# Optimization experiments

Measured on AMD Instinct MI355X. Metric: run time of the kernel, lower is better.

## Reference

```python
import jax, jax.numpy as jnp
import numpy as np

DIM = 70      # voxel grid side
NE = 6        # element channels
B = 8         # batch
TARGET = 29   # TARGET_NUM in source


def _xavier(key, shape, fan_in, fan_out):
    lim = float(np.sqrt(6.0 / (fan_in + fan_out)))
    return jax.random.uniform(key, shape, jnp.float32, -lim, lim)


def setup_inputs() -> dict:
    key = jax.random.key(0)
    ks = jax.random.split(key, 12)
    # Sparse binary occupancy grid: ~34 atoms per channel per molecule.
    x = (jax.random.uniform(ks[0], (B, NE, DIM, DIM, DIM)) < 1e-4).astype(jnp.float32)
    sigma = 2.0 * jnp.ones((NE,), jnp.float32)
    k3 = 3 * 3 * 3
    conv1_w = _xavier(ks[1], (32, NE, 3, 3, 3), NE * k3, 32 * k3)
    conv2_w = _xavier(ks[2], (64, 32, 3, 3, 3), 32 * k3, 64 * k3)
    conv3_w = _xavier(ks[3], (128, 64, 3, 3, 3), 64 * k3, 128 * k3)
    conv4_w = _xavier(ks[4], (256, 128, 3, 3, 3), 128 * k3, 256 * k3)
    conv1_b = jnp.full((32,), 0.01, jnp.float32)
    conv2_b = jnp.full((64,), 0.01, jnp.float32)
    conv3_b = jnp.full((128,), 0.01, jnp.float32)
    conv4_b = jnp.full((256,), 0.01, jnp.float32)
    fc1_w = _xavier(ks[5], (1024, 2048), 2048, 1024)
    fc1_b = jnp.full((1024,), 0.01, jnp.float32)
    fc2_w = _xavier(ks[6], (TARGET, 1024), 1024, TARGET)
    fc2_b = jax.random.uniform(ks[7], (TARGET,), jnp.float32, -1.0 / 32.0, 1.0 / 32.0)
    return dict(x=x, sigma=sigma,
                conv1_w=conv1_w, conv1_b=conv1_b, conv2_w=conv2_w, conv2_b=conv2_b,
                conv3_w=conv3_w, conv3_b=conv3_b, conv4_w=conv4_w, conv4_b=conv4_b,
                fc1_w=fc1_w, fc1_b=fc1_b, fc2_w=fc2_w, fc2_b=fc2_b)


def _blur(x, sigma):
    # Faithful to source: Gaussian centered at raw voxel INDICES (x0,y0,z0 from
    # nonzero()) but evaluated on SHIFTED coords arange(-dim/2, dim/2).
    # Separable Gaussian -> three 1D contractions instead of per-atom loops.
    coords = jnp.arange(DIM, dtype=jnp.float32) - DIM / 2.0   # -35 .. 34
    idx = jnp.arange(DIM, dtype=jnp.float32)                   # 0 .. 69
    d2 = (coords[:, None] - idx[None, :]) ** 2                 # [70,70]
    G = jnp.exp(-d2[None, :, :] / (2.0 * sigma[:, None, None] ** 2))  # [e,out,in]
    mask = (x != 0).astype(x.dtype)                            # [b,e,i,j,k]
    t = jnp.einsum('beijk,eai->beajk', mask, G)
    t = jnp.einsum('beajk,epj->beapk', t, G)
    cube = jnp.einsum('beapk,eqk->beapq', t, G)                # [b,e,70,70,70]
    return cube


def _conv3d(h, w, b):
    y = jax.lax.conv_general_dilated(h, w, (1, 1, 1), 'VALID',
                                     dimension_numbers=('NCDHW', 'OIDHW', 'NCDHW'))
    return y + b[None, :, None, None, None]


def _pool(h):
    return jax.lax.reduce_window(h, -jnp.inf, jax.lax.max,
                                 (1, 1, 2, 2, 2), (1, 1, 2, 2, 2), 'VALID')


def reference(x, sigma, conv1_w, conv1_b, conv2_w, conv2_b, conv3_w, conv3_b,
              conv4_w, conv4_b, fc1_w, fc1_b, fc2_w, fc2_b):
    h = _blur(x, sigma)
    h = jax.nn.relu(_pool(_conv3d(h, conv1_w, conv1_b)))
    h = jax.nn.relu(_pool(_conv3d(h, conv2_w, conv2_b)))
    h = jax.nn.relu(_pool(_conv3d(h, conv3_w, conv3_b)))
    h = jax.nn.relu(_pool(_conv3d(h, conv4_w, conv4_b)))  # [B,256,2,2,2]
    v = h.reshape(x.shape[0], -1)                          # [B,2048]
    y1 = jax.nn.relu(v @ fc1_w.T + fc1_b)
    y2 = y1 @ fc2_w.T + fc2_b                              # [B,29]
    return y2
```

## Files before the change

kernel.cpp:

```cpp
#include <hip/hip_runtime.h>
#include <hip/hip_bf16.h>

#define DIMV 70
#define NEL 6
#define BATCH 8

typedef unsigned short u16;
typedef unsigned int u32;
typedef __bf16 bf16x8 __attribute__((ext_vector_type(8)));
typedef short short8v __attribute__((ext_vector_type(8)));
typedef float f32x4 __attribute__((ext_vector_type(4)));

__device__ __forceinline__ u16 f2bf(float f) {
  __hip_bfloat16 h = __float2bfloat16(f);
  return __builtin_bit_cast(u16, h);
}
__device__ __forceinline__ float bf2f(u16 u) {
  unsigned int x = ((unsigned int)u) << 16;
  return __builtin_bit_cast(float, x);
}

__global__ __launch_bounds__(256) void k_zero(float* __restrict__ p, int n4) {
  int i = blockIdx.x * 256 + threadIdx.x;
  if (i < n4) ((float4*)p)[i] = make_float4(0.f, 0.f, 0.f, 0.f);
}

__global__ __launch_bounds__(256) void k_scan(const float* __restrict__ x,
                                              int* __restrict__ cnt,
                                              int* __restrict__ lists) {
  const int N4 = (BATCH * NEL * DIMV * DIMV * DIMV) / 4;
  int i = blockIdx.x * 256 + threadIdx.x;
  if (i >= N4) return;
  float4 v = ((const float4*)x)[i];
  int ch = i / 85750;
  int local = 4 * i - ch * 343000;
  float f[4] = {v.x, v.y, v.z, v.w};
#pragma unroll
  for (int k = 0; k < 4; ++k) {
    if (f[k] != 0.f) {
      int slot = atomicAdd(&cnt[ch], 1);
      if (slot < 512) lists[ch * 512 + slot] = local + k;
    }
  }
}

__global__ __launch_bounds__(256) void k_gather(const int* __restrict__ cnt,
                                                const int* __restrict__ lists,
                                                const float* __restrict__ sigma,
                                                u32* __restrict__ cube, int b0) {
  const int z = blockIdx.x;
  const int bl = blockIdx.y / NEL;
  const int e = blockIdx.y % NEL;
  const int chG = (b0 + bl) * NEL + e;
  const int tid = threadIdx.x;
  float sg = sigma[e];
  float inv2s2 = 1.f / (2.f * sg * sg);

  __shared__ int s_n;
  __shared__ int s_idx[512];
  __shared__ float s_wz[512];
  __shared__ float s_wy[32 * 70];
  __shared__ float s_wx[32 * 70];

  if (tid == 0) s_n = 0;
  __syncthreads();
  int n = min(cnt[chG], 512);
  for (int t = tid; t < n; t += 256) {
    int idx = lists[chG * 512 + t];
    int i0 = idx / 4900;
    float d = (float)(z - 35 - i0);
    float wz = expf(-d * d * inv2s2);
    if (wz > 1e-30f) {
      int s = atomicAdd(&s_n, 1);
      s_idx[s] = idx;
      s_wz[s] = wz;
    }
  }
  __syncthreads();
  int m = s_n;

  float acc[20];
#pragma unroll
  for (int k = 0; k < 20; ++k) acc[k] = 0.f;

  for (int t0 = 0; t0 < m; t0 += 32) {
    int tn = min(32, m - t0);
    __syncthreads();
    for (int u = tid; u < tn * 70; u += 256) {
      int t = u / 70, pos = u % 70;
      int idx = s_idx[t0 + t];
      int j0 = (idx / 70) % 70, k0 = idx % 70;
      float dy = (float)(pos - 35 - j0);
      float dx = (float)(pos - 35 - k0);
      s_wy[t * 70 + pos] = s_wz[t0 + t] * expf(-dy * dy * inv2s2);
      s_wx[t * 70 + pos] = expf(-dx * dx * inv2s2);
    }
    __syncthreads();
#pragma unroll
    for (int k = 0; k < 20; ++k) {
      int v = tid + k * 256;
      if (v < 4900) {
        int y = v / 70, xx = v % 70;
        float a = 0.f;
        for (int t = 0; t < tn; ++t)
          a = fmaf(s_wy[t * 70 + y], s_wx[t * 70 + xx], a);
        acc[k] += a;
      }
    }
  }
  size_t base = ((size_t)(bl * NEL + e) * DIMV + z) * 4900;
#pragma unroll
  for (int k = 0; k < 20; ++k) {
    int v = tid + k * 256;
    if (v < 4900) {
      float val = acc[k];
      u16 hi = f2bf(val);
      u16 lo = f2bf(val - bf2f(hi));
      cube[base + v] = ((u32)hi << 16) | (u32)lo;
    }
  }
}

__global__ __launch_bounds__(256) void k_pack_c1d(const float* __restrict__ w,
                                                  u16* __restrict__ Ah,
                                                  u16* __restrict__ Al) {
  int idx = blockIdx.x * 256 + threadIdx.x;
  if (idx >= 32 * 224) return;
  int o = idx / 224, k = idx % 224;
  int kk = k >> 5, r = k & 31;
  int g = r >> 3, e = r & 7;
  int off = 4 * kk + g;
  u16 h = 0, l = 0;
  if (off < 27 && e < 6) {
    float wv = w[(o * 6 + e) * 27 + off];
    u16 hi = f2bf(wv);
    h = hi;
    l = f2bf(wv - bf2f(hi));
  }
  Ah[idx] = h;
  Al[idx] = l;
}

__global__ __launch_bounds__(256) void k_pack_s(const float* __restrict__ w,
                                                u16* __restrict__ A,
                                                int CINL, int COUT) {
  int K2 = CINL * 81;
  int idx = blockIdx.x * 256 + threadIdx.x;
  if (idx >= COUT * K2) return;
  int o = idx / K2, k = idx % K2;
  int kb = k >> 5, r = k & 31;
  int g = r >> 3, e = r & 7;
  int kk = kb % 27;
  int t = kb / 27;
  int snum = CINL >> 5;
  int sub = t % snum, s = t / snum;
  int c = sub * 32 + 8 * g + e;
  float wv = w[(o * CINL + c) * 27 + kk];
  u16 hi = f2bf(wv);
  A[idx] = (s == 2) ? f2bf(wv - bf2f(hi)) : hi;
}

__global__ __launch_bounds__(256) void k_conv1(
    const u16* __restrict__ Ah, const u16* __restrict__ Al,
    const u32* __restrict__ cube, const float* __restrict__ bias,
    float* __restrict__ out, int b0) {
  __shared__ __align__(16) u16 Thi[1120 * 8];
  __shared__ __align__(16) u16 Tlo[1120 * 8];
  const int tid = threadIdx.x;
  const int wave = tid >> 6, lane = tid & 63;
  const int n = lane & 15, g = lane >> 4;
  const int py = blockIdx.x % 34, pz = blockIdx.x / 34;
  const int blb = blockIdx.y, bG = blb + b0;

  u32* thw = (u32*)Thi;
  u32* tlw = (u32*)Tlo;
  for (int i = tid; i < 4480; i += 256) {
    int j = i & 3, pos = i >> 2;
    int xx = pos % 70, line = pos / 70;
    int z = 2 * pz + (line >> 2), y = 2 * py + (line & 3);
    u32 a = 0, b2 = 0;
    if (j < 3) {
      size_t p0 = (((size_t)(blb * 6 + 2 * j) * 70 + z) * 70 + y) * 70 + xx;
      a = cube[p0];
      b2 = cube[p0 + 343000];
    }
    thw[pos * 4 + j] = (a >> 16) | (b2 & 0xFFFF0000u);
    tlw[pos * 4 + j] = (a & 0xFFFFu) | (b2 << 16);
  }
  __syncthreads();

  const int rc = wave;
  f32x4 acc[2][5] = {};
  for (int kk = 0; kk < 7; ++kk) {
    bf16x8 a0[2], a2[2];
#pragma unroll
    for (int mt = 0; mt < 2; ++mt) {
      const u16* bp = (const u16*)0;
      a0[mt] = __builtin_bit_cast(
          bf16x8, *(const short8v*)(Ah + (size_t)(mt * 16 + n) * 224 + kk * 32 + 8 * g));
      a2[mt] = __builtin_bit_cast(
          bf16x8, *(const short8v*)(Al + (size_t)(mt * 16 + n) * 224 + kk * 32 + 8 * g));
      (void)bp;
    }
    int off = min(4 * kk + g, 26);
    int dz = off / 9, dy = (off / 3) % 3, dx = off % 3;
    int line = ((rc >> 1) + dz) * 4 + (rc & 1) + dy;
#pragma unroll
    for (int nt = 0; nt < 5; ++nt) {
      int x_in = nt * 16 + n + dx;
      if (x_in > 69) x_in = 69;
      int cell = (line * 70 + x_in) * 8;
      bf16x8 bh = __builtin_bit_cast(bf16x8, *(const short8v*)&Thi[cell]);
      bf16x8 bl = __builtin_bit_cast(bf16x8, *(const short8v*)&Tlo[cell]);
#pragma unroll
      for (int mt = 0; mt < 2; ++mt) {
        acc[mt][nt] = __builtin_amdgcn_mfma_f32_16x16x32_bf16(a0[mt], bh, acc[mt][nt], 0, 0, 0);
        acc[mt][nt] = __builtin_amdgcn_mfma_f32_16x16x32_bf16(a2[mt], bh, acc[mt][nt], 0, 0, 0);
        acc[mt][nt] = __builtin_amdgcn_mfma_f32_16x16x32_bf16(a0[mt], bl, acc[mt][nt], 0, 0, 0);
      }
    }
  }
  __syncthreads();
  float* Pb = (float*)Thi;
#pragma unroll
  for (int mt = 0; mt < 2; ++mt) {
#pragma unroll
    for (int nt = 0; nt < 5; ++nt) {
#pragma unroll
      for (int r = 0; r < 4; ++r) {
        float v = acc[mt][nt][r];
        float v2 = fmaxf(v, __shfl_xor(v, 1));
        int o = mt * 16 + 4 * g + r;
        int px = (nt * 16 + n) >> 1;
        if (!(n & 1) && px < 34) Pb[(wave * 32 + o) * 34 + px] = v2;
      }
    }
  }
  __syncthreads();
  for (int t = tid; t < 1088; t += 256) {
    int o = t / 34, px = t % 34;
    float m = fmaxf(fmaxf(Pb[t], Pb[1088 + t]), fmaxf(Pb[2176 + t], Pb[3264 + t]));
    float rv = fmaxf(m + bias[o], 0.f);
    out[((((size_t)bG * 32 + o) * 34 + pz) * 34 + py) * 34 + px] = rv;
  }
}

template <int CINL, int COUT, int DIN, int WAVES, int MREP, int XT>
__global__ __launch_bounds__(WAVES * 64) void k_conv_s(
    const u16* __restrict__ Apack, const float* __restrict__ in,
    const float* __restrict__ bias, float* __restrict__ out) {
  constexpr int DP = (DIN - 2) / 2;
  constexpr int SNUM = CINL / 32;
  constexpr int K2 = 81 * CINL;
  __shared__ __align__(16) u16 T[16 * DIN * 32];

  const int tid = threadIdx.x;
  const int wave = tid >> 6, lane = tid & 63;
  const int n = lane & 15, g = lane >> 4;
  const int py = blockIdx.x % DP, pz = blockIdx.x / DP;
  const int b = blockIdx.y;

  f32x4 acc[MREP][4][XT] = {};

  for (int ph = 0; ph < 2; ++ph) {
    for (int sub = 0; sub < SNUM; ++sub) {
      if (ph + sub) __syncthreads();
      const int E2 = 16 * DIN * 16;
      for (int i = tid; i < E2; i += WAVES * 64) {
        int xx = i % DIN;
        int t2 = i / DIN;
        int jp = t2 & 15;
        int line = t2 >> 4;
        int z = 2 * pz + (line >> 2), y = 2 * py + (line & 3);
        int c = sub * 32 + 2 * jp;
        size_t base = (((size_t)(b * CINL + c) * DIN + z) * DIN + y) * DIN + xx;
        float v0 = in[base];
        float v1 = in[base + (size_t)DIN * DIN * DIN];
        u16 h0 = f2bf(v0), h1 = f2bf(v1);
        u16 a0 = ph ? f2bf(v0 - bf2f(h0)) : h0;
        u16 a1 = ph ? f2bf(v1 - bf2f(h1)) : h1;
        int byte = (line * DIN + xx) * 64 + (((jp >> 2) ^ (xx & 3)) << 4) + ((jp & 3) << 2);
        *(u32*)((char*)T + byte) = (u32)a0 | ((u32)a1 << 16);
      }
      __syncthreads();
      for (int kk = 0; kk < 27; ++kk) {
        bf16x8 a0[MREP], a2[MREP];
#pragma unroll
        for (int mr = 0; mr < MREP; ++mr) {
          int mtile = wave + WAVES * mr;
          const u16* base = Apack + (size_t)(mtile * 16 + n) * K2 + 8 * g;
          if (ph == 0) {
            a0[mr] = __builtin_bit_cast(
                bf16x8, *(const short8v*)(base + ((0 * SNUM + sub) * 27 + kk) * 32));
            a2[mr] = __builtin_bit_cast(
                bf16x8, *(const short8v*)(base + ((2 * SNUM + sub) * 27 + kk) * 32));
          } else {
            a0[mr] = __builtin_bit_cast(
                bf16x8, *(const short8v*)(base + ((1 * SNUM + sub) * 27 + kk) * 32));
          }
        }
        int dz = kk / 9, dy = (kk / 3) % 3, dx = kk % 3;
#pragma unroll
        for (int rc = 0; rc < 4; ++rc) {
          int line = ((rc >> 1) + dz) * 4 + (rc & 1) + dy;
#pragma unroll
          for (int nt = 0; nt < XT; ++nt) {
            int x_in = nt * 16 + n + dx;
            if (x_in > DIN - 1) x_in = DIN - 1;
            int byte = (line * DIN + x_in) * 64 + ((g ^ (x_in & 3)) << 4);
            bf16x8 bfr = __builtin_bit_cast(bf16x8, *(const short8v*)((const char*)T + byte));
#pragma unroll
            for (int mr = 0; mr < MREP; ++mr) {
              acc[mr][rc][nt] =
                  __builtin_amdgcn_mfma_f32_16x16x32_bf16(a0[mr], bfr, acc[mr][rc][nt], 0, 0, 0);
              if (ph == 0)
                acc[mr][rc][nt] = __builtin_amdgcn_mfma_f32_16x16x32_bf16(
                    a2[mr], bfr, acc[mr][rc][nt], 0, 0, 0);
            }
          }
        }
      }
    }
  }
#pragma unroll
  for (int mr = 0; mr < MREP; ++mr) {
    int mtile = wave + WAVES * mr;
#pragma unroll
    for (int nt = 0; nt < XT; ++nt) {
#pragma unroll
      for (int r = 0; r < 4; ++r) {
        float v = fmaxf(fmaxf(acc[mr][0][nt][r], acc[mr][1][nt][r]),
                        fmaxf(acc[mr][2][nt][r], acc[mr][3][nt][r]));
        float v2 = fmaxf(v, __shfl_xor(v, 1));
        int o = mtile * 16 + 4 * g + r;
        int px = (nt * 16 + n) >> 1;
        if (!(n & 1) && px < DP) {
          float rv = fmaxf(v2 + bias[o], 0.f);
          out[((((size_t)b * COUT + o) * DP + pz) * DP + py) * DP + px] = rv;
        }
      }
    }
  }
}

__global__ __launch_bounds__(512) void k_conv4ks(
    const u16* __restrict__ Apack, const float* __restrict__ in,
    float* __restrict__ P) {
  __shared__ __align__(16) u16 T[343 * 32];
  const int tid = threadIdx.x;
  const int wave = tid >> 6, lane = tid & 63;
  const int n = lane & 15, g = lane >> 4;
  const int q = blockIdx.x;
  const int third = q >> 3;
  const int r8 = q & 7;
  const int ph = r8 >> 2, sub = r8 & 3;
  const int b = blockIdx.y;

  for (int i = tid; i < 343 * 16; i += 512) {
    int jp = i & 15, pos = i >> 4;
    int c = sub * 32 + 2 * jp;
    const float* src = in + (size_t)(b * 128 + c) * 343 + pos;
    float v0 = src[0];
    float v1 = src[343];
    u16 h0 = f2bf(v0), h1 = f2bf(v1);
    u16 a0 = ph ? f2bf(v0 - bf2f(h0)) : h0;
    u16 a1 = ph ? f2bf(v1 - bf2f(h1)) : h1;
    int byte = pos * 64 + (((jp >> 2) ^ (pos & 3)) << 4) + ((jp & 3) << 2);
    *(u32*)((char*)T + byte) = (u32)a0 | ((u32)a1 << 16);
  }
  __syncthreads();

  f32x4 acc[2][4] = {};
  const int ys = n >> 2, xo = n & 3;
  for (int t = 0; t < 9; ++t) {
    int kk = third * 9 + t;
    int dz = kk / 9, dy = (kk / 3) % 3, dx = kk % 3;
    bf16x8 a0[2], a2[2];
#pragma unroll
    for (int mr = 0; mr < 2; ++mr) {
      int mtile = wave + 8 * mr;
      const u16* base = Apack + (size_t)(mtile * 16 + n) * 10368 + 8 * g;
      if (ph == 0) {
        a0[mr] = __builtin_bit_cast(
            bf16x8, *(const short8v*)(base + ((0 * 4 + sub) * 27 + kk) * 32));
        a2[mr] = __builtin_bit_cast(
            bf16x8, *(const short8v*)(base + ((2 * 4 + sub) * 27 + kk) * 32));
      } else {
        a0[mr] = __builtin_bit_cast(
            bf16x8, *(const short8v*)(base + ((1 * 4 + sub) * 27 + kk) * 32));
      }
    }
    int ybase = (ys + dy) * 7 + xo + dx;
#pragma unroll
    for (int zr = 0; zr < 4; ++zr) {
      int pos = (zr + dz) * 49 + ybase;
      int byte = pos * 64 + ((g ^ (pos & 3)) << 4);
      bf16x8 bfr = __builtin_bit_cast(bf16x8, *(const short8v*)((const char*)T + byte));
#pragma unroll
      for (int mr = 0; mr < 2; ++mr) {
        acc[mr][zr] = __builtin_amdgcn_mfma_f32_16x16x32_bf16(a0[mr], bfr, acc[mr][zr], 0, 0, 0);
        if (ph == 0)
          acc[mr][zr] = __builtin_amdgcn_mfma_f32_16x16x32_bf16(a2[mr], bfr, acc[mr][zr], 0, 0, 0);
      }
    }
  }
  float* Pq = P + (size_t)(q * 8 + b) * 16384;
#pragma unroll
  for (int mr = 0; mr < 2; ++mr) {
    int mtile = wave + 8 * mr;
#pragma unroll
    for (int zr = 0; zr < 4; ++zr) {
#pragma unroll
      for (int r = 0; r < 4; ++r) {
        int o = mtile * 16 + 4 * g + r;
        Pq[o * 64 + zr * 16 + n] = acc[mr][zr][r];
      }
    }
  }
}

__global__ __launch_bounds__(256) void k_fin4(const float* __restrict__ P,
                                              const float* __restrict__ bias,
                                              float* __restrict__ h4) {
  int t = blockIdx.x * 256 + threadIdx.x;
  if (t >= 16384) return;
  int w = t & 7;
  int o = (t >> 3) & 255;
  int b = t >> 11;
  int pd = w >> 2, p2 = (w >> 1) & 1, pw = w & 1;
  float m = -1e30f;
#pragma unroll
  for (int dz = 0; dz < 2; ++dz)
#pragma unroll
    for (int dy = 0; dy < 2; ++dy)
#pragma unroll
      for (int dx = 0; dx < 2; ++dx) {
        int pos = (2 * pd + dz) * 16 + (2 * p2 + dy) * 4 + (2 * pw + dx);
        float s = 0.f;
        for (int q = 0; q < 24; ++q)
          s += P[(size_t)(q * 8 + b) * 16384 + o * 64 + pos];
        m = fmaxf(m, s);
      }
  h4[(size_t)b * 2048 + o * 8 + w] = fmaxf(m + bias[o], 0.f);
}

__global__ __launch_bounds__(64) void k_fc1(const float* __restrict__ v,
                                            const float* __restrict__ W,
                                            const float* __restrict__ bias,
                                            float* __restrict__ y) {
  int o = blockIdx.x;
  int lane = threadIdx.x;
  float acc[8] = {};
  for (int k = lane; k < 2048; k += 64) {
    float wv = W[o * 2048 + k];
#pragma unroll
    for (int bb = 0; bb < 8; ++bb)
      acc[bb] = fmaf(v[bb * 2048 + k], wv, acc[bb]);
  }
#pragma unroll
  for (int off = 32; off; off >>= 1)
#pragma unroll
    for (int bb = 0; bb < 8; ++bb) acc[bb] += __shfl_xor(acc[bb], off);
  if (lane == 0) {
    float bo = bias[o];
#pragma unroll
    for (int bb = 0; bb < 8; ++bb) y[bb * 1024 + o] = fmaxf(acc[bb] + bo, 0.f);
  }
}

__global__ __launch_bounds__(64) void k_fc2(const float* __restrict__ v,
                                            const float* __restrict__ W,
                                            const float* __restrict__ bias,
                                            float* __restrict__ y) {
  int o = blockIdx.x;
  int lane = threadIdx.x;
  float acc[8] = {};
  for (int k = lane; k < 1024; k += 64) {
    float wv = W[o * 1024 + k];
#pragma unroll
    for (int bb = 0; bb < 8; ++bb)
      acc[bb] = fmaf(v[bb * 1024 + k], wv, acc[bb]);
  }
#pragma unroll
  for (int off = 32; off; off >>= 1)
#pragma unroll
    for (int bb = 0; bb < 8; ++bb) acc[bb] += __shfl_xor(acc[bb], off);
  if (lane == 0) {
    float bo = bias[o];
#pragma unroll
    for (int bb = 0; bb < 8; ++bb) y[bb * 29 + o] = acc[bb] + bo;
  }
}

extern "C" void kernel_launch(void* const* d_in, const int* in_sizes, int n_in,
                              void* d_out, int out_size, void* d_ws, size_t ws_size,
                              hipStream_t stream) {
  const float* x   = (const float*)d_in[0];
  const float* sig = (const float*)d_in[1];
  const float* w1  = (const float*)d_in[2];
  const float* b1  = (const float*)d_in[3];
  const float* w2  = (const float*)d_in[4];
  const float* b2  = (const float*)d_in[5];
  const float* w3  = (const float*)d_in[6];
  const float* b3  = (const float*)d_in[7];
  const float* w4  = (const float*)d_in[8];
  const float* b4  = (const float*)d_in[9];
  const float* fw1 = (const float*)d_in[10];
  const float* fb1 = (const float*)d_in[11];
  const float* fw2 = (const float*)d_in[12];
  const float* fb2 = (const float*)d_in[13];

  char* ws = (char*)d_ws;
  u32*   cube4 = (u32*)(ws + 0);
  float* P     = (float*)(ws + 0);
  float* h1    = (float*)(ws + 32928000);
  u16*   ah1   = (u16*)(ws + 73200000);
  u16*   al1   = (u16*)(ws + 73250000);
  u16*   ap2   = (u16*)(ws + 73300000);
  u16*   ap3   = (u16*)(ws + 73700000);
  u16*   ap4   = (u16*)(ws + 75100000);
  float* h2    = (float*)(ws + 80500000);
  float* h3    = (float*)(ws + 89000000);
  float* h4    = (float*)(ws + 90500000);
  float* y1    = (float*)(ws + 90600000);
  int*   cnt   = (int*)(ws + 90700000);
  int*   lists = (int*)(ws + 90701024);

  k_pack_c1d<<<(32 * 224 + 255) / 256, 256, 0, stream>>>(w1, ah1, al1);
  k_pack_s<<<(64 * 2592 + 255) / 256, 256, 0, stream>>>(w2, ap2, 32, 64);
  k_pack_s<<<(128 * 5184 + 255) / 256, 256, 0, stream>>>(w3, ap3, 64, 128);
  k_pack_s<<<(256 * 10368 + 255) / 256, 256, 0, stream>>>(w4, ap4, 128, 256);

  k_zero<<<1, 256, 0, stream>>>((float*)cnt, 12);
  const int N4 = (BATCH * NEL * DIMV * DIMV * DIMV) / 4;
  k_scan<<<(N4 + 255) / 256, 256, 0, stream>>>(x, cnt, lists);

  for (int half = 0; half < 2; ++half) {
    int b0 = 4 * half;
    k_gather<<<dim3(DIMV, 4 * NEL), 256, 0, stream>>>(cnt, lists, sig, cube4, b0);
    k_conv1<<<dim3(34 * 34, 4), 256, 0, stream>>>(ah1, al1, cube4, b1, h1, b0);
  }

  k_conv_s<32,  64, 34, 4, 1, 2><<<dim3(16 * 16, 8), 256, 0, stream>>>(ap2, h1, b2, h2);
  k_conv_s<64, 128, 16, 8, 1, 1><<<dim3(7 * 7, 8),   512, 0, stream>>>(ap3, h2, b3, h3);

  k_conv4ks<<<dim3(24, 8), 512, 0, stream>>>(ap4, h3, P);
  k_fin4<<<64, 256, 0, stream>>>(P, b4, h4);

  k_fc1<<<1024, 64, 0, stream>>>(h4, fw1, fb1, y1);
  k_fc2<<<29, 64, 0, stream>>>(y1, fw2, fb2, (float*)d_out);
}
```

Measured before the change: 561.0 us.

## Split conv2/conv3 waves by output row instead of output-channel tile

In k_conv_s, each wave used to own one output-channel tile and loop over all four (z,y) row combinations of the pool window. Now each wave owns a single row combination and several channel tiles (MREP derived from COUT and wave groups). The 2x2 pool across rows is done through a shared-memory staging buffer before bias, ReLU and store. The LDS swizzle also changes from x&3 to (x>>1)&3 to cut bank conflicts. This changes how weight loads and LDS B-fragment reads are reused, at the cost of an extra shared-memory pass and two more barriers.

```diff
diff --git a/kernel.cpp b/kernel.cpp
--- a/kernel.cpp
+++ b/kernel.cpp
@@ -195,12 +195,10 @@
     bf16x8 a0[2], a2[2];
 #pragma unroll
     for (int mt = 0; mt < 2; ++mt) {
-      const u16* bp = (const u16*)0;
       a0[mt] = __builtin_bit_cast(
           bf16x8, *(const short8v*)(Ah + (size_t)(mt * 16 + n) * 224 + kk * 32 + 8 * g));
       a2[mt] = __builtin_bit_cast(
           bf16x8, *(const short8v*)(Al + (size_t)(mt * 16 + n) * 224 + kk * 32 + 8 * g));
-      (void)bp;
     }
     int off = min(4 * kk + g, 26);
     int dz = off / 9, dy = (off / 3) % 3, dx = off % 3;
@@ -245,13 +243,15 @@
   }
 }
 
-template <int CINL, int COUT, int DIN, int WAVES, int MREP, int XT>
+template <int CINL, int COUT, int DIN, int WAVES, int XT>
 __global__ __launch_bounds__(WAVES * 64) void k_conv_s(
     const u16* __restrict__ Apack, const float* __restrict__ in,
     const float* __restrict__ bias, float* __restrict__ out) {
   constexpr int DP = (DIN - 2) / 2;
   constexpr int SNUM = CINL / 32;
   constexpr int K2 = 81 * CINL;
+  constexpr int OG = WAVES / 4;
+  constexpr int MREP = COUT / (16 * OG);
   __shared__ __align__(16) u16 T[16 * DIN * 32];
 
   const int tid = threadIdx.x;
@@ -259,8 +259,9 @@
   const int n = lane & 15, g = lane >> 4;
   const int py = blockIdx.x % DP, pz = blockIdx.x / DP;
   const int b = blockIdx.y;
-
-  f32x4 acc[MREP][4][XT] = {};
+  const int rc = wave & 3, og = wave >> 2;
+
+  f32x4 acc[MREP][XT] = {};
 
   for (int ph = 0; ph < 2; ++ph) {
     for (int sub = 0; sub < SNUM; ++sub) {
@@ -279,7 +280,7 @@
         u16 h0 = f2bf(v0), h1 = f2bf(v1);
         u16 a0 = ph ? f2bf(v0 - bf2f(h0)) : h0;
         u16 a1 = ph ? f2bf(v1 - bf2f(h1)) : h1;
-        int byte = (line * DIN + xx) * 64 + (((jp >> 2) ^ (xx & 3)) << 4) + ((jp & 3) << 2);
+        int byte = (line * DIN + xx) * 64 + ((((jp >> 2) ^ ((xx >> 1) & 3))) << 4) + ((jp & 3) << 2);
         *(u32*)((char*)T + byte) = (u32)a0 | ((u32)a1 << 16);
       }
       __syncthreads();
@@ -287,7 +288,7 @@
         bf16x8 a0[MREP], a2[MREP];
 #pragma unroll
         for (int mr = 0; mr < MREP; ++mr) {
-          int mtile = wave + WAVES * mr;
+          int mtile = og * MREP + mr;
           const u16* base = Apack + (size_t)(mtile * 16 + n) * K2 + 8 * g;
           if (ph == 0) {
             a0[mr] = __builtin_bit_cast(
@@ -300,46 +301,49 @@
           }
         }
         int dz = kk / 9, dy = (kk / 3) % 3, dx = kk % 3;
-#pragma unroll
-        for (int rc = 0; rc < 4; ++rc) {
-          int line = ((rc >> 1) + dz) * 4 + (rc & 1) + dy;
-#pragma unroll
-          for (int nt = 0; nt < XT; ++nt) {
-            int x_in = nt * 16 + n + dx;
-            if (x_in > DIN - 1) x_in = DIN - 1;
-            int byte = (line * DIN + x_in) * 64 + ((g ^ (x_in & 3)) << 4);
-            bf16x8 bfr = __builtin_bit_cast(bf16x8, *(const short8v*)((const char*)T + byte));
-#pragma unroll
-            for (int mr = 0; mr < MREP; ++mr) {
-              acc[mr][rc][nt] =
-                  __builtin_amdgcn_mfma_f32_16x16x32_bf16(a0[mr], bfr, acc[mr][rc][nt], 0, 0, 0);
-              if (ph == 0)
-                acc[mr][rc][nt] = __builtin_amdgcn_mfma_f32_16x16x32_bf16(
-                    a2[mr], bfr, acc[mr][rc][nt], 0, 0, 0);
-            }
+        int line = ((rc >> 1) + dz) * 4 + (rc & 1) + dy;
+#pragma unroll
+        for (int nt = 0; nt < XT; ++nt) {
+          int x_in = nt * 16 + n + dx;
+          if (x_in > DIN - 1) x_in = DIN - 1;
+          int byte = (line * DIN + x_in) * 64 + ((g ^ ((x_in >> 1) & 3)) << 4);
+          bf16x8 bfr = __builtin_bit_cast(bf16x8, *(const short8v*)((const char*)T + byte));
+#pragma unroll
+          for (int mr = 0; mr < MREP; ++mr) {
+            acc[mr][nt] =
+                __builtin_amdgcn_mfma_f32_16x16x32_bf16(a0[mr], bfr, acc[mr][nt], 0, 0, 0);
+            if (ph == 0)
+              acc[mr][nt] =
+                  __builtin_amdgcn_mfma_f32_16x16x32_bf16(a2[mr], bfr, acc[mr][nt], 0, 0, 0);
           }
         }
       }
     }
   }
+  __syncthreads();
+  float* Pb = (float*)T;
 #pragma unroll
   for (int mr = 0; mr < MREP; ++mr) {
-    int mtile = wave + WAVES * mr;
+    int mtile = og * MREP + mr;
 #pragma unroll
     for (int nt = 0; nt < XT; ++nt) {
 #pragma unroll
       for (int r = 0; r < 4; ++r) {
-        float v = fmaxf(fmaxf(acc[mr][0][nt][r], acc[mr][1][nt][r]),
-                        fmaxf(acc[mr][2][nt][r], acc[mr][3][nt][r]));
+        float v = acc[mr][nt][r];
         float v2 = fmaxf(v, __shfl_xor(v, 1));
         int o = mtile * 16 + 4 * g + r;
         int px = (nt * 16 + n) >> 1;
-        if (!(n & 1) && px < DP) {
-          float rv = fmaxf(v2 + bias[o], 0.f);
-          out[((((size_t)b * COUT + o) * DP + pz) * DP + py) * DP + px] = rv;
-        }
-      }
-    }
+        if (!(n & 1) && px < DP) Pb[(rc * COUT + o) * DP + px] = v2;
+      }
+    }
+  }
+  __syncthreads();
+  for (int t = tid; t < COUT * DP; t += WAVES * 64) {
+    int o = t / DP, px = t % DP;
+    float m = fmaxf(fmaxf(Pb[t], Pb[COUT * DP + t]),
+                    fmaxf(Pb[2 * COUT * DP + t], Pb[3 * COUT * DP + t]));
+    float rv = fmaxf(m + bias[o], 0.f);
+    out[((((size_t)b * COUT + o) * DP + pz) * DP + py) * DP + px] = rv;
   }
 }
 
@@ -541,8 +545,8 @@
     k_conv1<<<dim3(34 * 34, 4), 256, 0, stream>>>(ah1, al1, cube4, b1, h1, b0);
   }
 
-  k_conv_s<32,  64, 34, 4, 1, 2><<<dim3(16 * 16, 8), 256, 0, stream>>>(ap2, h1, b2, h2);
-  k_conv_s<64, 128, 16, 8, 1, 1><<<dim3(7 * 7, 8),   512, 0, stream>>>(ap3, h2, b3, h3);
+  k_conv_s<32,  64, 34, 4, 2><<<dim3(16 * 16, 8), 256, 0, stream>>>(ap2, h1, b2, h2);
+  k_conv_s<64, 128, 16, 8, 1><<<dim3(7 * 7, 8),   512, 0, stream>>>(ap3, h2, b3, h3);
 
   k_conv4ks<<<dim3(24, 8), 512, 0, stream>>>(ap4, h3, P);
   k_fin4<<<64, 256, 0, stream>>>(P, b4, h4);
```

After: 874.9 us. 56.0% more time.
